# Optimization experiments

Hardware: AMD Instinct MI355X
Metric: run time of the kernel (lower is better)

The kernel has to match this reference:

```python
import jax, jax.numpy as jnp
import numpy as np

HIDDEN = 128
N_NODES = 50000
N_EDGES = 600000


def setup_inputs() -> dict:
    key = jax.random.key(0)
    k_h, k_s, k_d, k_w1, k_b1, k_w2, k_b2 = jax.random.split(key, 7)
    h = jax.random.normal(k_h, (N_NODES, HIDDEN), dtype=jnp.float32)
    src = jax.random.randint(k_s, (N_EDGES,), 0, N_NODES, dtype=jnp.int64)
    dst = jax.random.randint(k_d, (N_EDGES,), 0, N_NODES, dtype=jnp.int64)
    # link_predictor params: Linear(2H -> H), Linear(H -> 1)
    lim1 = 1.0 / np.sqrt(2 * HIDDEN)
    W1 = jax.random.uniform(k_w1, (2 * HIDDEN, HIDDEN), dtype=jnp.float32, minval=-lim1, maxval=lim1)
    b1 = jax.random.uniform(k_b1, (HIDDEN,), dtype=jnp.float32, minval=-lim1, maxval=lim1)
    lim2 = 1.0 / np.sqrt(HIDDEN)
    W2 = jax.random.uniform(k_w2, (HIDDEN, 1), dtype=jnp.float32, minval=-lim2, maxval=lim2)
    b2 = jax.random.uniform(k_b2, (1,), dtype=jnp.float32, minval=-lim2, maxval=lim2)
    return {"h": h, "W1": W1, "b1": b1, "W2": W2, "b2": b2, "src": src, "dst": dst}


def reference(h, W1, b1, W2, b2, src, dst):
    # per-edge gather of source/destination node features, concat -> [E, 2H]
    h_cat = jnp.concatenate([h[src], h[dst]], axis=1)
    hid = jax.nn.relu(h_cat @ W1 + b1)           # [E, H]
    score = jax.nn.sigmoid(hid @ W2 + b2)        # [E, 1]
    return score.squeeze(-1)                     # [E]
```

## Files before the change

### kernel.cpp

```cpp
#include <hip/hip_runtime.h>
#include <hip/hip_bf16.h>


#define HID    128
#define NNODE  50000
#define NEDGE  600000
#define NGRP   ((NNODE + 31) / 32)
#define K1BLK  ((NGRP + 1) / 2)
#define K2BLK  2048
#define UVBYTES ((size_t)NNODE * 256 * 2)
#define WTFRAG_OFF UVBYTES

typedef __attribute__((ext_vector_type(8)))  __bf16 bf16x8;
typedef __attribute__((ext_vector_type(16))) float  f32x16;

static __device__ __forceinline__ unsigned int pack2bf(float a, float b) {
    unsigned int ua = __float_as_uint(a);
    unsigned int ub = __float_as_uint(b);
    ua = (ua + 0x7FFFu + ((ua >> 16) & 1u)) >> 16;
    ub = (ub + 0x7FFFu + ((ub >> 16) & 1u)) >> 16;
    return (ub << 16) | (ua & 0xFFFFu);
}

__global__ __launch_bounds__(256, 1) void w1_frag_kernel(
    const float* __restrict__ W1, unsigned short* __restrict__ w1tf)
{
    const int T = blockIdx.x * 256 + threadIdx.x;
    const int l31  = T & 31;
    const int FIDX = T >> 5;
    const int l5 = FIDX & 1, ks = (FIDX >> 1) & 7;
    const int ct = (FIDX >> 4) & 3, colhalf = FIDX >> 6;
    const int kb = colhalf * 128 + ks * 16 + l5 * 8;
    const int n  = ct * 32 + l31;
    bf16x8 v;
#pragma unroll
    for (int j = 0; j < 8; ++j) v[j] = (__bf16)W1[(kb + j) * HID + n];
    *(bf16x8*)(w1tf + (size_t)T * 8) = v;
}

__global__ __launch_bounds__(256, 3) void node_gemm_kernel(
    const float* __restrict__ h, const unsigned short* __restrict__ w1tf,
    const float* __restrict__ b1, unsigned short* __restrict__ uvs)
{
    const int t = threadIdx.x, lane = t & 63, wv = t >> 6;
    const int l31 = lane & 31, l5 = lane >> 5;

    const int group = blockIdx.x * 2 + (wv >> 1);
    if (group >= NGRP) return;
    const int colhalf = wv & 1;

    float b1v[4];
#pragma unroll
    for (int ct = 0; ct < 4; ++ct)
        b1v[ct] = (colhalf == 0) ? b1[ct * 32 + l31] : 0.0f;

    const int node  = group * 32 + l31;
    const int nodec = node < NNODE ? node : NNODE - 1;
    const float* hp = h + (size_t)nodec * HID + l5 * 8;

    f32x16 acc[4];
#pragma unroll
    for (int ct = 0; ct < 4; ++ct)
#pragma unroll
        for (int r = 0; r < 16; ++r) acc[ct][r] = 0.0f;

#pragma unroll
    for (int ks = 0; ks < 8; ++ks) {
        float4 f0 = *(const float4*)(hp + ks * 16);
        float4 f1 = *(const float4*)(hp + ks * 16 + 4);
        bf16x8 af;
        af[0] = (__bf16)f0.x; af[1] = (__bf16)f0.y;
        af[2] = (__bf16)f0.z; af[3] = (__bf16)f0.w;
        af[4] = (__bf16)f1.x; af[5] = (__bf16)f1.y;
        af[6] = (__bf16)f1.z; af[7] = (__bf16)f1.w;
#pragma unroll
        for (int ct = 0; ct < 4; ++ct) {
            const int fidx = ((colhalf * 4 + ct) * 8 + ks) * 2 + l5;
            bf16x8 bfg = *(const bf16x8*)(w1tf + (size_t)fidx * 256 + l31 * 8);
            acc[ct] = __builtin_amdgcn_mfma_f32_32x32x16_bf16(af, bfg,
                                                              acc[ct], 0, 0, 0);
        }
    }

#pragma unroll
    for (int ct = 0; ct < 4; ++ct) {
#pragma unroll
        for (int r = 0; r < 16; ++r) {
            float mine = acc[ct][r] + b1v[ct];
            float partner = __shfl_xor(mine, 1);
            if (!(l31 & 1)) {
                const int rr = (r & 3) + 8 * (r >> 2) + 4 * l5;
                const int nd = group * 32 + rr;
                if (nd < NNODE) {
                    const int n = colhalf * 128 + ct * 32 + l31;
                    *(unsigned int*)(uvs + (size_t)nd * 256 + n) =
                        pack2bf(mine, partner);
                }
            }
        }
    }
}

__global__ __launch_bounds__(256, 8) void edge_score_kernel(
    const unsigned short* __restrict__ uvs,
    const float* __restrict__ W2, const float* __restrict__ b2,
    const int* __restrict__ src, const int* __restrict__ dst,
    float* __restrict__ out)
{
    const int t = threadIdx.x, lane = t & 63, wv = t >> 6;
    const int c = lane & 15;
    const int g = lane >> 4;

    bool idx64;
    {
        unsigned long long m =
            __ballot((src[2 * lane + 1] == 0) && (dst[2 * lane + 1] == 0));
        idx64 = (m == ~0ULL);
    }

    float w2f[8];
#pragma unroll
    for (int j = 0; j < 8; ++j) w2f[j] = W2[c * 8 + j];
    const float b2s = b2[0];

    const int gw = blockIdx.x * 4 + wv;
    const int NW = K2BLK * 4;
    const int NQ = NEDGE / 4;

    for (int q0 = gw; q0 < NQ; q0 += 2 * NW) {
        const int q1  = q0 + NW;
        const int q1c = q1 < NQ ? q1 : NQ - 1;
        const int e0  = q0 * 4 + g;
        const int e1  = q1c * 4 + g;

        const int ns0 = idx64 ? src[2 * e0] : src[e0];
        const int nd0 = idx64 ? dst[2 * e0] : dst[e0];
        const int ns1 = idx64 ? src[2 * e1] : src[e1];
        const int nd1 = idx64 ? dst[2 * e1] : dst[e1];

        const uint4 qu0 = *(const uint4*)(uvs + (size_t)ns0 * 256 + c * 8);
        const uint4 qv0 = *(const uint4*)(uvs + (size_t)nd0 * 256 + 128 + c * 8);
        const uint4 qu1 = *(const uint4*)(uvs + (size_t)ns1 * 256 + c * 8);
        const uint4 qv1 = *(const uint4*)(uvs + (size_t)nd1 * 256 + 128 + c * 8);

#pragma unroll
        for (int half = 0; half < 2; ++half) {
            const uint4 qu = half ? qu1 : qu0;
            const uint4 qv = half ? qv1 : qv0;
            float p = 0.0f;
#pragma unroll
            for (int j = 0; j < 4; ++j) {
                const unsigned int uw = j == 0 ? qu.x : j == 1 ? qu.y
                                      : j == 2 ? qu.z : qu.w;
                const unsigned int vw = j == 0 ? qv.x : j == 1 ? qv.y
                                      : j == 2 ? qv.z : qv.w;
                float slo = __uint_as_float(uw << 16)
                          + __uint_as_float(vw << 16);
                float shi = __uint_as_float(uw & 0xFFFF0000u)
                          + __uint_as_float(vw & 0xFFFF0000u);
                slo = slo > 0.0f ? slo : 0.0f;
                shi = shi > 0.0f ? shi : 0.0f;
                p = fmaf(slo, w2f[2 * j], p);
                p = fmaf(shi, w2f[2 * j + 1], p);
            }
            p += __shfl_xor(p, 1);
            p += __shfl_xor(p, 2);
            p += __shfl_xor(p, 4);
            p += __shfl_xor(p, 8);

            if (c == 0 && (half == 0 || q1 < NQ)) {
                const int e = half ? e1 : e0;
                out[e] = 1.0f / (1.0f + __expf(-(p + b2s)));
            }
        }
    }
}

__global__ __launch_bounds__(256, 1) void edge_mlp_fallback(
    const float* __restrict__ h,  const float* __restrict__ W1,
    const float* __restrict__ b1, const float* __restrict__ W2,
    const float* __restrict__ b2, const int* __restrict__ src,
    const int* __restrict__ dst,  float* __restrict__ out)
{
    __shared__ unsigned char smem[65536];
    const int t = threadIdx.x, lane = t & 63, wv = t >> 6;
    const int l31 = lane & 31, l5 = lane >> 5;
    bool idx64;
    {
        unsigned long long m =
            __ballot((src[2 * lane + 1] == 0) && (dst[2 * lane + 1] == 0));
        idx64 = (m == ~0ULL);
    }
    for (int task = t; task < 4096; task += 256) {
        int n = task & 127, slot = task >> 7;
        const float* wp = W1 + (slot * 8) * HID + n;
        bf16x8 v;
#pragma unroll
        for (int j = 0; j < 8; ++j) v[j] = (__bf16)wp[j * HID];
        *(bf16x8*)(smem + n * 512 + ((slot * 16) ^ ((n & 31) << 4))) = v;
    }
    float b1v[4], w2v[4];
#pragma unroll
    for (int ct = 0; ct < 4; ++ct) {
        int n = ct * 32 + l31;
        b1v[ct] = b1[n]; w2v[ct] = W2[n];
    }
    const float b2s = b2[0];
    __syncthreads();
    const int swz = l31 << 4;
    const int gw = blockIdx.x * 4 + wv;
    for (int tile = gw; tile < NEDGE / 32; tile += 512 * 4) {
        const int e = tile * 32 + l31;
        const long long ns = idx64 ? (long long)src[2 * e] : (long long)src[e];
        const long long nd = idx64 ? (long long)dst[2 * e] : (long long)dst[e];
        const float* hs = h + ns * HID + l5 * 8;
        const float* hd = h + nd * HID + l5 * 8;
        f32x16 acc[4];
#pragma unroll
        for (int ct = 0; ct < 4; ++ct)
#pragma unroll
            for (int r = 0; r < 16; ++r) acc[ct][r] = 0.0f;
#pragma unroll
        for (int ks = 0; ks < 16; ++ks) {
            const float* p = (ks < 8) ? (hs + ks * 16) : (hd + (ks - 8) * 16);
            float4 f0 = *(const float4*)p;
            float4 f1 = *(const float4*)(p + 4);
            bf16x8 af;
            af[0] = (__bf16)f0.x; af[1] = (__bf16)f0.y;
            af[2] = (__bf16)f0.z; af[3] = (__bf16)f0.w;
            af[4] = (__bf16)f1.x; af[5] = (__bf16)f1.y;
            af[6] = (__bf16)f1.z; af[7] = (__bf16)f1.w;
            const int coff = ks * 32 + l5 * 16;
#pragma unroll
            for (int ct = 0; ct < 4; ++ct) {
                const int n = ct * 32 + l31;
                bf16x8 bfg = *(const bf16x8*)(smem + n * 512 + (coff ^ swz));
                acc[ct] = __builtin_amdgcn_mfma_f32_32x32x16_bf16(af, bfg,
                                                                  acc[ct], 0, 0, 0);
            }
        }
        float p[16];
#pragma unroll
        for (int r = 0; r < 16; ++r) p[r] = 0.0f;
#pragma unroll
        for (int ct = 0; ct < 4; ++ct)
#pragma unroll
            for (int r = 0; r < 16; ++r) {
                float v = acc[ct][r] + b1v[ct];
                v = v > 0.0f ? v : 0.0f;
                p[r] += v * w2v[ct];
            }
#pragma unroll
        for (int r = 0; r < 16; ++r) {
            p[r] += __shfl_xor(p[r], 1);  p[r] += __shfl_xor(p[r], 2);
            p[r] += __shfl_xor(p[r], 4);  p[r] += __shfl_xor(p[r], 8);
            p[r] += __shfl_xor(p[r], 16);
        }
        if (l31 == 0) {
#pragma unroll
            for (int g = 0; g < 4; ++g) {
                const int e0 = tile * 32 + g * 8 + l5 * 4;
                float4 o4;
                o4.x = 1.0f / (1.0f + __expf(-(p[4 * g + 0] + b2s)));
                o4.y = 1.0f / (1.0f + __expf(-(p[4 * g + 1] + b2s)));
                o4.z = 1.0f / (1.0f + __expf(-(p[4 * g + 2] + b2s)));
                o4.w = 1.0f / (1.0f + __expf(-(p[4 * g + 3] + b2s)));
                *(float4*)(out + e0) = o4;
            }
        }
    }
}

extern "C" void kernel_launch(void* const* d_in, const int* in_sizes, int n_in,
                              void* d_out, int out_size, void* d_ws, size_t ws_size,
                              hipStream_t stream) {
    const float* h  = (const float*)d_in[0];
    const float* W1 = (const float*)d_in[1];
    const float* b1 = (const float*)d_in[2];
    const float* W2 = (const float*)d_in[3];
    const float* b2 = (const float*)d_in[4];
    const int* src  = (const int*)d_in[5];
    const int* dst  = (const int*)d_in[6];
    (void)in_sizes; (void)n_in; (void)out_size;

    const size_t need = WTFRAG_OFF + 65536;
    if (ws_size >= need) {
        unsigned short* uvs  = (unsigned short*)d_ws;
        unsigned short* w1tf = (unsigned short*)((char*)d_ws + WTFRAG_OFF);
        w1_frag_kernel<<<16, 256, 0, stream>>>(W1, w1tf);
        node_gemm_kernel<<<K1BLK, 256, 0, stream>>>(h, w1tf, b1, uvs);
        edge_score_kernel<<<K2BLK, 256, 0, stream>>>(uvs, W2, b2, src, dst,
                                                     (float*)d_out);
    } else {
        edge_mlp_fallback<<<512, 256, 0, stream>>>(h, W1, b1, W2, b2, src, dst,
                                                   (float*)d_out);
    }
}
```

Measured before the change: 76.24 us.

## Stage node features in swizzled LDS and split column tiles across four waves

The node GEMM now processes one 32-node group per block. The block loads and converts the h rows to bf16 once into XOR-swizzled shared memory, and each of four waves computes two of the eight 32-column tiles. Before, each wave loaded its own h fragments from global memory, so two waves read the same rows redundantly. Halving the accumulators per wave and launching twice as many blocks is meant to raise parallelism, at the cost of a block-wide barrier, 8 KB of LDS per block, and a lower launch-bounds occupancy hint.

```diff
diff --git a/kernel.cpp b/kernel.cpp
--- a/kernel.cpp
+++ b/kernel.cpp
@@ -6,7 +6,6 @@
 #define NNODE  50000
 #define NEDGE  600000
 #define NGRP   ((NNODE + 31) / 32)
-#define K1BLK  ((NGRP + 1) / 2)
 #define K2BLK  2048
 #define UVBYTES ((size_t)NNODE * 256 * 2)
 #define WTFRAG_OFF UVBYTES
@@ -38,61 +37,84 @@
     *(bf16x8*)(w1tf + (size_t)T * 8) = v;
 }
 
-__global__ __launch_bounds__(256, 3) void node_gemm_kernel(
+__global__ __launch_bounds__(256, 2) void node_gemm_kernel(
     const float* __restrict__ h, const unsigned short* __restrict__ w1tf,
     const float* __restrict__ b1, unsigned short* __restrict__ uvs)
 {
+    __shared__ unsigned char smem[8192];
+
     const int t = threadIdx.x, lane = t & 63, wv = t >> 6;
     const int l31 = lane & 31, l5 = lane >> 5;
-
-    const int group = blockIdx.x * 2 + (wv >> 1);
-    if (group >= NGRP) return;
-    const int colhalf = wv & 1;
-
-    float b1v[4];
-#pragma unroll
-    for (int ct = 0; ct < 4; ++ct)
-        b1v[ct] = (colhalf == 0) ? b1[ct * 32 + l31] : 0.0f;
-
-    const int node  = group * 32 + l31;
-    const int nodec = node < NNODE ? node : NNODE - 1;
-    const float* hp = h + (size_t)nodec * HID + l5 * 8;
-
-    f32x16 acc[4];
-#pragma unroll
-    for (int ct = 0; ct < 4; ++ct)
-#pragma unroll
-        for (int r = 0; r < 16; ++r) acc[ct][r] = 0.0f;
+    const int group = blockIdx.x;
+
+    {
+        const float* hb = h + (size_t)group * 32 * HID;
+        const bool tail = (group == NGRP - 1);
+#pragma unroll
+        for (int it = 0; it < 2; ++it) {
+            const int tau = it * 256 + t;
+            const int r = tau >> 4, s = tau & 15;
+            const float* src_;
+            if (tail) {
+                const int node = group * 32 + r;
+                const int rc = (node < NNODE) ? r : (NNODE - 1 - group * 32);
+                src_ = hb + rc * HID + s * 8;
+            } else {
+                src_ = hb + tau * 8;
+            }
+            float4 f0 = *(const float4*)src_;
+            float4 f1 = *(const float4*)(src_ + 4);
+            bf16x8 v;
+            v[0] = (__bf16)f0.x; v[1] = (__bf16)f0.y;
+            v[2] = (__bf16)f0.z; v[3] = (__bf16)f0.w;
+            v[4] = (__bf16)f1.x; v[5] = (__bf16)f1.y;
+            v[6] = (__bf16)f1.z; v[7] = (__bf16)f1.w;
+            *(bf16x8*)(smem + r * 256 + ((s * 16) ^ ((r & 7) << 4))) = v;
+        }
+    }
+    __syncthreads();
+
+    const int colhalf = wv >> 1;
+    const int ctpair  = wv & 1;
+
+    float b1v[2];
+#pragma unroll
+    for (int cc = 0; cc < 2; ++cc)
+        b1v[cc] = (colhalf == 0) ? b1[(ctpair * 2 + cc) * 32 + l31] : 0.0f;
+
+    f32x16 acc[2];
+#pragma unroll
+    for (int cc = 0; cc < 2; ++cc)
+#pragma unroll
+        for (int r = 0; r < 16; ++r) acc[cc][r] = 0.0f;
+
+    const int abase = l31 * 256;
+    const int aswz  = (l31 & 7) << 4;
 
 #pragma unroll
     for (int ks = 0; ks < 8; ++ks) {
-        float4 f0 = *(const float4*)(hp + ks * 16);
-        float4 f1 = *(const float4*)(hp + ks * 16 + 4);
-        bf16x8 af;
-        af[0] = (__bf16)f0.x; af[1] = (__bf16)f0.y;
-        af[2] = (__bf16)f0.z; af[3] = (__bf16)f0.w;
-        af[4] = (__bf16)f1.x; af[5] = (__bf16)f1.y;
-        af[6] = (__bf16)f1.z; af[7] = (__bf16)f1.w;
-#pragma unroll
-        for (int ct = 0; ct < 4; ++ct) {
-            const int fidx = ((colhalf * 4 + ct) * 8 + ks) * 2 + l5;
+        bf16x8 af = *(const bf16x8*)(smem + abase +
+                                     ((ks * 32 + l5 * 16) ^ aswz));
+#pragma unroll
+        for (int cc = 0; cc < 2; ++cc) {
+            const int fidx = ((colhalf * 4 + ctpair * 2 + cc) * 8 + ks) * 2 + l5;
             bf16x8 bfg = *(const bf16x8*)(w1tf + (size_t)fidx * 256 + l31 * 8);
-            acc[ct] = __builtin_amdgcn_mfma_f32_32x32x16_bf16(af, bfg,
-                                                              acc[ct], 0, 0, 0);
-        }
-    }
-
-#pragma unroll
-    for (int ct = 0; ct < 4; ++ct) {
+            acc[cc] = __builtin_amdgcn_mfma_f32_32x32x16_bf16(af, bfg,
+                                                              acc[cc], 0, 0, 0);
+        }
+    }
+
+#pragma unroll
+    for (int cc = 0; cc < 2; ++cc) {
 #pragma unroll
         for (int r = 0; r < 16; ++r) {
-            float mine = acc[ct][r] + b1v[ct];
+            float mine = acc[cc][r] + b1v[cc];
             float partner = __shfl_xor(mine, 1);
             if (!(l31 & 1)) {
                 const int rr = (r & 3) + 8 * (r >> 2) + 4 * l5;
                 const int nd = group * 32 + rr;
                 if (nd < NNODE) {
-                    const int n = colhalf * 128 + ct * 32 + l31;
+                    const int n = colhalf * 128 + (ctpair * 2 + cc) * 32 + l31;
                     *(unsigned int*)(uvs + (size_t)nd * 256 + n) =
                         pack2bf(mine, partner);
                 }
@@ -288,7 +310,7 @@
         unsigned short* uvs  = (unsigned short*)d_ws;
         unsigned short* w1tf = (unsigned short*)((char*)d_ws + WTFRAG_OFF);
         w1_frag_kernel<<<16, 256, 0, stream>>>(W1, w1tf);
-        node_gemm_kernel<<<K1BLK, 256, 0, stream>>>(h, w1tf, b1, uvs);
+        node_gemm_kernel<<<NGRP, 256, 0, stream>>>(h, w1tf, b1, uvs);
         edge_score_kernel<<<K2BLK, 256, 0, stream>>>(uvs, W2, b2, src, dst,
                                                      (float*)d_out);
     } else {
```

After: 67.05 us, median of 2. -12.1%, faster.
